# Kernel optimization log

Hardware: AMD Instinct MI355X
Metric: run time of the kernel (lower is better)

The kernel has to match this reference:

```python
import jax, jax.numpy as jnp
import numpy as np

CODEBOOK_SIZE = 4096
EMBED_DIM = 256
BETA = 0.25


def setup_inputs() -> dict:
    key = jax.random.key(0)
    k_z, k_cb = jax.random.split(key)
    z = jax.random.normal(k_z, (32, 256, 32, 32), dtype=jnp.float32)
    # nn.Embedding weight init: uniform(-1/D, 1/D)
    codebook = jax.random.uniform(
        k_cb, (CODEBOOK_SIZE, EMBED_DIM), dtype=jnp.float32,
        minval=-1.0 / EMBED_DIM, maxval=1.0 / EMBED_DIM)
    return {"z": z, "codebook": codebook}


def reference(z, codebook):
    b, c, h, w = z.shape
    # (B,C,H,W) -> (B*H*W, D)
    z_flat = jnp.transpose(z, (0, 2, 3, 1)).reshape(-1, c)
    # squared euclidean distances: ||z||^2 - 2 z.e^T + ||e||^2  (== cdist(...)^2)
    z_sq = jnp.sum(z_flat * z_flat, axis=1, keepdims=True)          # (N,1)
    e_sq = jnp.sum(codebook * codebook, axis=1)                     # (K,)
    distances = z_sq - 2.0 * (z_flat @ codebook.T) + e_sq[None, :]  # (N,K)
    min_encoding_indices = jnp.argmin(distances, axis=1)            # (N,)
    z_q_flat = codebook[min_encoding_indices]                       # (N,D)
    z_q = jnp.transpose(z_q_flat.reshape(b, h, w, c), (0, 3, 1, 2))  # (B,C,H,W)
    # straight-through estimator
    z_q_st = z + jax.lax.stop_gradient(z_q - z)
    codebook_loss = jnp.mean((z_q - jax.lax.stop_gradient(z)) ** 2)
    commitment_loss = jnp.mean((z - jax.lax.stop_gradient(z_q)) ** 2)
    vq_loss = codebook_loss + BETA * commitment_loss
    return (z_q_st, vq_loss, min_encoding_indices.reshape(b, h, w))
```

## Files before the change

### kernel.cpp

```cpp
#include <hip/hip_runtime.h>

#define K_CODES 4096
#define D 256
#define N_VEC 32768
#define N_ELEM 8388608
#define WINDOW 3.5e-4f
#define WINDOW_C 5.25e-4f
#define CAP 14
#define CSTRIDE 16
#define RG 8
#define RSLICE 256

typedef _Float16 f16x8 __attribute__((ext_vector_type(8)));
typedef float f32x4 __attribute__((ext_vector_type(4)));

#define WS_LOSS 0
#define WS_COUNT 8
#define WS_DONE 16
#define WS_COUNT2 24
#define WS_IDX 256
#define WS_LIST (WS_IDX + N_VEC * 4)
#define WS_ESQ (WS_LIST + N_VEC * 4)
#define WS_ZSQ (WS_ESQ + K_CODES * 4)
#define WS_APACK (WS_ZSQ + N_VEC * 4)
#define WS_BPACK (WS_APACK + (size_t)N_VEC * 256 * 2)
#define WS_RFIN (WS_BPACK + (size_t)K_CODES * 256 * 2 + 65536)
#define WS_ZT (WS_RFIN + (size_t)N_VEC * 8)
#define WS_NEED_ZT (WS_ZT + (size_t)N_VEC * D * 4)
#define WS_S1F WS_NEED_ZT
#define WS_CANDN (WS_S1F + (size_t)N_VEC * 4)
#define WS_CANDL (WS_CANDN + (size_t)N_VEC * 4)
#define WS_LISTB (WS_CANDL + (size_t)N_VEC * CSTRIDE * 2)
#define WS_NEED_CAND (WS_LISTB + (size_t)N_VEC * 4)

#define PREP_PZ 4096
#define PREP_PCB 512
#define PREP_ESQ 1024
#define PREP_ZSQ 128
#define PREP_BLOCKS (PREP_PZ + PREP_PCB + PREP_ESQ + PREP_ZSQ)

__device__ __forceinline__ unsigned long long pack_key(float s, int idx) {
  const unsigned u = __float_as_uint(s);
  const unsigned mk = (u & 0x80000000u) ? ~u : (u | 0x80000000u);
  return ((unsigned long long)mk << 12) | (unsigned long long)(unsigned)idx;
}
__device__ __forceinline__ float key_score(unsigned long long k) {
  const unsigned mk = (unsigned)(k >> 12);
  const unsigned u = (mk & 0x80000000u) ? (mk & 0x7fffffffu) : ~mk;
  return __uint_as_float(u);
}

__device__ __forceinline__ void pin_frag(f16x8& v) {
  asm volatile("" : "+v"(v));
}

__device__ void esq_body(int bx, const float* __restrict__ cb,
                         float* __restrict__ esq) {
  const int lane = threadIdx.x & 63;
  const int k = bx * 4 + (threadIdx.x >> 6);
  const float* row = cb + (size_t)k * D;
  double s = 0.;
#pragma unroll
  for (int j = 0; j < 4; ++j) {
    const float v = row[lane + 64 * j];
    s += (double)__fmul_rn(v, v);
  }
#pragma unroll
  for (int off = 32; off > 0; off >>= 1) s += __shfl_down(s, off, 64);
  if (lane == 0) esq[k] = (float)s;
}

__device__ void zsq_body(int bx, const float* __restrict__ z,
                         float* __restrict__ zsq) {
  const int n = bx * 256 + threadIdx.x;
  const int b = n >> 10;
  const int hw = n & 1023;
  const float* p = z + ((size_t)b << 18) + hw;
  double a0 = 0., a1 = 0., a2 = 0., a3 = 0.;
  for (int c = 0; c < D; c += 4) {
    const float v0 = p[(size_t)(c + 0) << 10];
    const float v1 = p[(size_t)(c + 1) << 10];
    const float v2 = p[(size_t)(c + 2) << 10];
    const float v3 = p[(size_t)(c + 3) << 10];
    a0 += (double)__fmul_rn(v0, v0);
    a1 += (double)__fmul_rn(v1, v1);
    a2 += (double)__fmul_rn(v2, v2);
    a3 += (double)__fmul_rn(v3, v3);
  }
  zsq[n] = (float)((a0 + a1) + (a2 + a3));
}

__device__ void pack_z2_body(int bx, const float* __restrict__ z,
                             _Float16* __restrict__ Ap,
                             float* __restrict__ zT) {
  const int t = bx * 256 + threadIdx.x;
  const int lane = t & 63;
  const int fid = t >> 6;
  const int ks = fid & 7;
  const int grp = fid >> 3;
  const int n = grp * 16 + (lane & 15);
  const int d = ks * 32 + ((lane >> 4) << 3);
  const int b = n >> 10, hw = n & 1023;
  const float* p = z + ((size_t)b << 18) + ((size_t)d << 10) + hw;
  float v[8];
  f16x8 H;
#pragma unroll
  for (int j = 0; j < 8; ++j) {
    v[j] = p[(size_t)j << 10];
    H[j] = (_Float16)v[j];
  }
  *(f16x8*)(Ap + (size_t)t * 8) = H;
  if (zT) {
    float4* o = (float4*)(zT + (size_t)n * D + d);
    o[0] = make_float4(v[0], v[1], v[2], v[3]);
    o[1] = make_float4(v[4], v[5], v[6], v[7]);
  }
}

__device__ void pack_cb2_body(int bx, const float* __restrict__ cb,
                              _Float16* __restrict__ Bp) {
  const int t = bx * 256 + threadIdx.x;
  const int lane = t & 63;
  const int fid = t >> 6;
  const int ks = fid & 7;
  const int grp = fid >> 3;
  const int k = grp * 16 + (lane & 15);
  const int d = ks * 32 + ((lane >> 4) << 3);
  const float* p = cb + (size_t)k * D + d;
  f16x8 H;
#pragma unroll
  for (int j = 0; j < 8; ++j) H[j] = (_Float16)(p[j] * 256.f);
  *(f16x8*)(Bp + (size_t)t * 8) = H;
}

__global__ __launch_bounds__(256) void prep_kernel(
    const float* __restrict__ z, const float* __restrict__ cb,
    float* __restrict__ esq, float* __restrict__ zsq,
    _Float16* __restrict__ Ap, _Float16* __restrict__ Bp,
    float* __restrict__ zT) {
  const int b = blockIdx.x;
  if (b < PREP_PZ) {
    pack_z2_body(b, z, Ap, zT);
  } else if (b < PREP_PZ + PREP_PCB) {
    pack_cb2_body(b - PREP_PZ, cb, Bp);
  } else if (b < PREP_PZ + PREP_PCB + PREP_ESQ) {
    esq_body(b - PREP_PZ - PREP_PCB, cb, esq);
  } else {
    zsq_body(b - PREP_PZ - PREP_PCB - PREP_ESQ, z, zsq);
  }
}

__global__ __launch_bounds__(512, 2) void dist2_kernel(
    const _Float16* __restrict__ Ap, const _Float16* __restrict__ Bp,
    const float* __restrict__ esq, int* __restrict__ idx,
    int* __restrict__ list, unsigned int* __restrict__ count,
    unsigned long long* __restrict__ rfin, float* __restrict__ s1f,
    int* __restrict__ listB, unsigned int* __restrict__ count2) {
  __shared__ unsigned long long mb[128][4][2];
  const int tid = threadIdx.x;
  const int lane = tid & 63;
  const int w = tid >> 6;
  const int wn = w >> 2;
  const int wc = w & 3;
  const int n0 = blockIdx.x * 128;

  f16x8 a[4][8];
  {
    const _Float16* ab =
        Ap + (size_t)((n0 + wn * 64) >> 4) * 4096 + (size_t)lane * 8;
#pragma unroll
    for (int ni = 0; ni < 4; ++ni)
#pragma unroll
      for (int ks = 0; ks < 8; ++ks) {
        a[ni][ks] = *(const f16x8*)(ab + (size_t)(ni * 8 + ks) * 512);
        pin_frag(a[ni][ks]);
      }
  }

  float s1[4], s2[4];
  int i1[4];
#pragma unroll
  for (int ni = 0; ni < 4; ++ni) {
    s1[ni] = 3.4e38f;
    s2[ni] = 3.4e38f;
    i1[ni] = 0;
  }

  const _Float16* bbase = Bp + (size_t)wc * 4096 + (size_t)lane * 8;
  const int crow = wc * 16 + ((lane >> 4) << 2);
  const f32x4 z4 = (f32x4)0.f;

  f16x8 b[8];
#pragma unroll
  for (int ks = 0; ks < 8; ++ks)
    b[ks] = *(const f16x8*)(bbase + (size_t)ks * 512);

  for (int t = 0; t < 64; ++t) {
    const float4 e4 = *(const float4*)(esq + t * 64 + crow);
    f32x4 acc0, acc1, acc2, acc3;
    __builtin_amdgcn_s_setprio(1);
#pragma unroll
    for (int ks = 0; ks < 8; ++ks) {
      acc0 = __builtin_amdgcn_mfma_f32_16x16x32_f16(b[ks], a[0][ks],
                                                    ks ? acc0 : z4, 0, 0, 0);
      acc1 = __builtin_amdgcn_mfma_f32_16x16x32_f16(b[ks], a[1][ks],
                                                    ks ? acc1 : z4, 0, 0, 0);
      acc2 = __builtin_amdgcn_mfma_f32_16x16x32_f16(b[ks], a[2][ks],
                                                    ks ? acc2 : z4, 0, 0, 0);
      acc3 = __builtin_amdgcn_mfma_f32_16x16x32_f16(b[ks], a[3][ks],
                                                    ks ? acc3 : z4, 0, 0, 0);
      b[ks] = *(const f16x8*)(bbase + (size_t)(t + 1) * 16384 + ks * 512);
    }
    __builtin_amdgcn_s_setprio(0);
    const int cb0 = t * 64 + crow;
    const float ev[4] = {e4.x, e4.y, e4.z, e4.w};
    f32x4 accv[4] = {acc0, acc1, acc2, acc3};
#pragma unroll
    for (int r = 0; r < 4; ++r) {
      const int code = cb0 + r;
#pragma unroll
      for (int ni = 0; ni < 4; ++ni) {
        const float s = fmaf(accv[ni][r], -0.0078125f, ev[r]);
        s2[ni] = fminf(fmaxf(s, s1[ni]), s2[ni]);
        if (s < s1[ni]) i1[ni] = code;
        s1[ni] = fminf(s1[ni], s);
      }
    }
  }

  unsigned long long k1[4], k2[4];
#pragma unroll
  for (int ni = 0; ni < 4; ++ni) {
    float a1 = s1[ni], a2 = s2[ni];
    int ai1 = i1[ni];
#pragma unroll
    for (int m = 16; m <= 32; m <<= 1) {
      const float bv1 = __shfl_xor(a1, m, 64);
      const int bi1 = __shfl_xor(ai1, m, 64);
      const float bv2 = __shfl_xor(a2, m, 64);
      const float hi = fmaxf(a1, bv1);
      const bool take = (bv1 < a1) || (bv1 == a1 && bi1 < ai1);
      if (take) ai1 = bi1;
      a1 = fminf(a1, bv1);
      a2 = fminf(fminf(a2, bv2), hi);
    }
    k1[ni] = pack_key(a1, ai1);
    k2[ni] = pack_key(a2, 0);
  }
  if (lane < 16) {
#pragma unroll
    for (int ni = 0; ni < 4; ++ni) {
      const int nl = wn * 64 + ni * 16 + lane;
      mb[nl][wc][0] = k1[ni];
      mb[nl][wc][1] = k2[ni];
    }
  }
  __syncthreads();
  if (tid < 128) {
    unsigned long long m1 = ~0ull, m2 = ~0ull;
#pragma unroll
    for (int s = 0; s < 4; ++s) {
      const unsigned long long c1 = mb[tid][s][0];
      const unsigned long long c2 = mb[tid][s][1];
      if (c1 < m1) {
        m2 = m1;
        m1 = c1;
      } else if (c1 < m2) {
        m2 = c1;
      }
      if (c2 < m2) m2 = c2;
    }
    const int n = n0 + tid;
    idx[n] = (int)(m1 & 0xFFFULL);
    const float sc0 = key_score(m1);
    if (s1f) s1f[n] = sc0;
    const bool flag = key_score(m2) - sc0 < WINDOW;
    rfin[n] = flag ? ~0ull : 0ull;
    if (flag) {
      if (s1f) {
        const unsigned pos = atomicAdd(count, 1u);
        if (pos < N_VEC) list[pos] = n;
      } else {
        const unsigned p2 = atomicAdd(count2, 1u);
        if (p2 < N_VEC) listB[p2] = n;
      }
    }
  }
}

__global__ __launch_bounds__(64) void certify_kernel(
    const _Float16* __restrict__ Ap, const _Float16* __restrict__ Bp,
    const float* __restrict__ esq, const float* __restrict__ s1f,
    const int* __restrict__ list, const unsigned int* __restrict__ count,
    unsigned int* __restrict__ candn, unsigned short* __restrict__ candl) {
  if (!candn) return;
  unsigned int cN = *count;
  if (cN > N_VEC) cN = N_VEC;
  if (cN == 0) return;
  const int lane = threadIdx.x & 63;
  const int l16 = lane & 15;
  const int quad = lane >> 4;
  const unsigned ptiles = (cN + 15) / 16;
  const unsigned items = ptiles * 16;
  const f32x4 z4 = (f32x4)0.f;
  for (unsigned item = blockIdx.x; item < items; item += gridDim.x) {
    const unsigned pt = item >> 4;
    const unsigned sl = item & 15;
    unsigned r = pt * 16 + l16;
    const bool valid = (r < cN);
    if (!valid) r = cN - 1;
    const int n = list[r];
    const float thr = s1f[n] + WINDOW_C;
    f16x8 af[8];
    const _Float16* ab = Ap + (size_t)(n >> 4) * 4096 + (size_t)quad * 128 +
                         (size_t)(n & 15) * 8;
#pragma unroll
    for (int ks = 0; ks < 8; ++ks) {
      af[ks] = *(const f16x8*)(ab + (size_t)ks * 512);
      pin_frag(af[ks]);
    }
#pragma unroll 2
    for (int g = 0; g < 16; ++g) {
      const int grp = sl * 16 + g;
      const _Float16* bb = Bp + (size_t)grp * 4096 + (size_t)lane * 8;
      f16x8 bf[8];
#pragma unroll
      for (int ks = 0; ks < 8; ++ks)
        bf[ks] = *(const f16x8*)(bb + (size_t)ks * 512);
      f32x4 acc;
#pragma unroll
      for (int ks = 0; ks < 8; ++ks)
        acc = __builtin_amdgcn_mfma_f32_16x16x32_f16(bf[ks], af[ks],
                                                     ks ? acc : z4, 0, 0, 0);
      const int cb0 = grp * 16 + quad * 4;
      const float4 e4 = *(const float4*)(esq + cb0);
      const float ev[4] = {e4.x, e4.y, e4.z, e4.w};
#pragma unroll
      for (int rr = 0; rr < 4; ++rr) {
        const float s = fmaf(acc[rr], -0.0078125f, ev[rr]);
        if (valid && s < thr) {
          const unsigned u = atomicAdd(&candn[n], 1u);
          if (u < CAP)
            candl[(size_t)n * CSTRIDE + u] = (unsigned short)(cb0 + rr);
        }
      }
    }
  }
}

__global__ __launch_bounds__(256) void rescanB_kernel(
    const float* __restrict__ zT, const float* __restrict__ cb,
    const float* __restrict__ esq, const float* __restrict__ zsq,
    const int* __restrict__ list, const unsigned int* __restrict__ count,
    const unsigned int* __restrict__ candn,
    const unsigned short* __restrict__ candl,
    unsigned long long* __restrict__ rfin, int* __restrict__ listB,
    unsigned int* __restrict__ count2) {
  if (!candn) return;
  unsigned int cN = *count;
  if (cN > N_VEC) cN = N_VEC;
  const int tid = threadIdx.x;
  const int j8 = tid & 7;
  for (unsigned i = blockIdx.x * 32 + (tid >> 3); i < cN;
       i += gridDim.x * 32) {
    const int n = list[i];
    const unsigned c = candn[n];
    if (c > CAP) {
      if (j8 == 0) {
        const unsigned p = atomicAdd(count2, 1u);
        if (p < N_VEC) listB[p] = n;
      }
      continue;
    }
    unsigned long long best = ~0ull;
    for (unsigned jj = j8; jj < c; jj += 8) {
      const int k = candl[(size_t)n * CSTRIDE + jj];
      const float* zr = zT + (size_t)n * D;
      const float* row = cb + (size_t)k * D;
      double a = 0.;
      for (int cc = 0; cc < D; cc += 4) {
        const float4 zf = *(const float4*)(zr + cc);
        const float4 r4 = *(const float4*)(row + cc);
        a = fma((double)zf.x, (double)r4.x, a);
        a = fma((double)zf.y, (double)r4.y, a);
        a = fma((double)zf.z, (double)r4.z, a);
        a = fma((double)zf.w, (double)r4.w, a);
      }
      const float d =
          __fadd_rn(__fsub_rn(zsq[n], __fmul_rn(2.0f, (float)a)), esq[k]);
      best = min(best, pack_key(d, k));
    }
    best = min(best, __shfl_xor(best, 1, 64));
    best = min(best, __shfl_xor(best, 2, 64));
    best = min(best, __shfl_xor(best, 4, 64));
    if (j8 == 0 && best != ~0ull) atomicMin(rfin + n, best);
  }
}

__global__ __launch_bounds__(256) void rescan_kernel(
    const float* __restrict__ z, const float* __restrict__ zT,
    const float* __restrict__ cb, const float* __restrict__ esq,
    const float* __restrict__ zsq, const int* __restrict__ list,
    const unsigned int* __restrict__ count,
    unsigned long long* __restrict__ rfin) {
  __shared__ double zrow[RG][D];
  __shared__ int nloc[RG];
  __shared__ float zsv[RG];
  const int tid = threadIdx.x;
  const int lane = tid & 63;
  unsigned int cnt = *count;
  if (cnt > N_VEC) cnt = N_VEC;
  const unsigned G = (cnt + RG - 1) / RG;
  const unsigned nitems = G * (K_CODES / RSLICE);
  for (unsigned item = blockIdx.x; item < nitems; item += gridDim.x) {
    const unsigned g = item >> 4;
    const int s = item & 15;
    __syncthreads();
    if (tid < RG) {
      const unsigned r = g * RG + tid;
      const int n = (r < cnt) ? list[r] : list[cnt - 1];
      nloc[tid] = n;
      zsv[tid] = zsq[n];
    }
    __syncthreads();
    if (zT) {
      for (int i = tid; i < RG * D; i += 256) {
        const int p = i >> 8, c = i & 255;
        zrow[p][c] = (double)zT[(size_t)nloc[p] * D + c];
      }
    } else {
      for (int i = tid; i < RG * D; i += 256) {
        const int p = i >> 8, c = i & 255;
        const int n = nloc[p];
        const int b = n >> 10, hw = n & 1023;
        zrow[p][c] = (double)z[((size_t)b << 18) + ((size_t)c << 10) + hw];
      }
    }
    __syncthreads();
    const int k = s * RSLICE + tid;
    const float* row = cb + (size_t)k * D;
    double acc[RG];
#pragma unroll
    for (int p = 0; p < RG; ++p) acc[p] = 0.;
    for (int c = 0; c < D; c += 4) {
      const float4 r4 = *(const float4*)(row + c);
      const double rx = (double)r4.x, ry = (double)r4.y;
      const double rz = (double)r4.z, rw = (double)r4.w;
#pragma unroll
      for (int p = 0; p < RG; ++p) {
        const double2 za = *(const double2*)&zrow[p][c];
        const double2 zb = *(const double2*)&zrow[p][c + 2];
        double a = acc[p];
        a = fma(za.x, rx, a);
        a = fma(za.y, ry, a);
        a = fma(zb.x, rz, a);
        a = fma(zb.y, rw, a);
        acc[p] = a;
      }
    }
    const float ek = esq[k];
    unsigned long long best[RG];
#pragma unroll
    for (int p = 0; p < RG; ++p) {
      const float dotf = (float)acc[p];
      const float d = __fadd_rn(__fsub_rn(zsv[p], __fmul_rn(2.0f, dotf)), ek);
      best[p] = pack_key(d, k);
    }
#pragma unroll
    for (int p = 0; p < RG; ++p) {
#pragma unroll
      for (int off = 32; off > 0; off >>= 1)
        best[p] = min(best[p], __shfl_down(best[p], off, 64));
    }
    if (lane == 0) {
#pragma unroll
      for (int p = 0; p < RG; ++p) atomicMin(rfin + nloc[p], best[p]);
    }
  }
}

__global__ __launch_bounds__(256) void gather_kernel(
    const float* __restrict__ z, const float* __restrict__ cb,
    const int* __restrict__ idxarr, const unsigned long long* __restrict__ rfin,
    float* __restrict__ out, float* __restrict__ loss_acc,
    unsigned int* __restrict__ done) {
  const int tid = threadIdx.x;
  const int n0 = blockIdx.x * 64;
  const int hwl = tid & 63;
  const int cq = tid >> 6;
  const int n = n0 + hwl;
  const int b = n >> 10;
  const int hw = n & 1023;
  const unsigned long long rf = rfin[n];
  const int idx = rf ? (int)(rf & 0xFFFULL) : idxarr[n];
  if (tid < 64) out[(size_t)N_ELEM + 1 + n] = (float)idx;
  const float* crow = cb + (size_t)idx * D;
  const size_t obase = ((size_t)b << 18) + hw;
  float part = 0.f;
#pragma unroll
  for (int j = 0; j < 16; ++j) {
    const int c = cq * 64 + j * 4;
    const float4 v4 = *(const float4*)(crow + c);
    const size_t o = obase + ((size_t)c << 10);
    const float d0 = v4.x - z[o];
    const float d1 = v4.y - z[o + 1024];
    const float d2 = v4.z - z[o + 2048];
    const float d3 = v4.w - z[o + 3072];
    out[o] = v4.x;
    out[o + 1024] = v4.y;
    out[o + 2048] = v4.z;
    out[o + 3072] = v4.w;
    part = fmaf(d0, d0, part);
    part = fmaf(d1, d1, part);
    part = fmaf(d2, d2, part);
    part = fmaf(d3, d3, part);
  }
#pragma unroll
  for (int off = 32; off > 0; off >>= 1) part += __shfl_down(part, off, 64);
  __shared__ float red[4];
  if ((tid & 63) == 0) red[tid >> 6] = part;
  __syncthreads();
  if (tid == 0) {
    atomicAdd(loss_acc, red[0] + red[1] + red[2] + red[3]);
    __threadfence();
    const unsigned old = atomicAdd(done, 1u);
    if (old == gridDim.x - 1) {
      const float total = atomicAdd(loss_acc, 0.0f);
      out[N_ELEM] = 1.25f * total * (1.0f / (float)N_ELEM);
    }
  }
}

extern "C" void kernel_launch(void* const* d_in, const int* in_sizes, int n_in,
                              void* d_out, int out_size, void* d_ws,
                              size_t ws_size, hipStream_t stream) {
  const float* z = (const float*)d_in[0];
  const float* cb = (const float*)d_in[1];
  float* out = (float*)d_out;
  char* ws = (char*)d_ws;
  float* loss_acc = (float*)(ws + WS_LOSS);
  unsigned int* count = (unsigned int*)(ws + WS_COUNT);
  unsigned int* done = (unsigned int*)(ws + WS_DONE);
  unsigned int* count2 = (unsigned int*)(ws + WS_COUNT2);
  int* idx = (int*)(ws + WS_IDX);
  int* list = (int*)(ws + WS_LIST);
  float* esq = (float*)(ws + WS_ESQ);
  float* zsq = (float*)(ws + WS_ZSQ);
  _Float16* Ap = (_Float16*)(ws + WS_APACK);
  _Float16* Bp = (_Float16*)(ws + WS_BPACK);
  unsigned long long* rfin = (unsigned long long*)(ws + WS_RFIN);
  float* zT = (ws_size >= WS_NEED_ZT) ? (float*)(ws + WS_ZT) : nullptr;
  const bool canduse = (ws_size >= WS_NEED_CAND) && (zT != nullptr);
  float* s1f = canduse ? (float*)(ws + WS_S1F) : nullptr;
  unsigned int* candn = canduse ? (unsigned int*)(ws + WS_CANDN) : nullptr;
  unsigned short* candl = canduse ? (unsigned short*)(ws + WS_CANDL) : nullptr;
  int* listB = canduse ? (int*)(ws + WS_LISTB) : list;

  hipMemsetAsync(ws, 0, 256, stream);
  if (canduse) hipMemsetAsync(ws + WS_CANDN, 0, (size_t)N_VEC * 4, stream);
  prep_kernel<<<PREP_BLOCKS, 256, 0, stream>>>(z, cb, esq, zsq, Ap, Bp, zT);
  dist2_kernel<<<N_VEC / 128, 512, 0, stream>>>(Ap, Bp, esq, idx, list, count,
                                                rfin, s1f, listB, count2);
  certify_kernel<<<2048, 64, 0, stream>>>(Ap, Bp, esq, s1f, list, count, candn,
                                          candl);
  rescanB_kernel<<<256, 256, 0, stream>>>(zT, cb, esq, zsq, list, count, candn,
                                          candl, rfin, listB, count2);
  rescan_kernel<<<2048, 256, 0, stream>>>(z, zT, cb, esq, zsq, listB, count2,
                                          rfin);
  gather_kernel<<<N_VEC / 64, 256, 0, stream>>>(z, cb, idx, rfin, out,
                                                loss_acc, done);
}
```

Measured before the change: 249.0 us.

## Fuse candidate certification and exact rescan into one block-local kernel

Replaces the separate certify, rescanB and rescan kernels with a single cresolve kernel. Each block takes 16 ambiguous vectors, recomputes their approximate fp16 MFMA distances against the whole codebook, and collects near-minimum candidates in shared memory. It then resolves them exactly in double precision, falling back to a full in-block scan when a vector has too many candidates. This removes the zT transpose buffer, the global candidate arrays and their memset, atomics, and extra launches, but each block now does all 4096-code MFMA work serially and can hit a costly full-scan path.

```diff
diff --git a/kernel.cpp b/kernel.cpp
--- a/kernel.cpp
+++ b/kernel.cpp
@@ -6,8 +6,7 @@
 #define N_ELEM 8388608
 #define WINDOW 3.5e-4f
 #define WINDOW_C 5.25e-4f
-#define CAP 14
-#define CSTRIDE 16
+#define CAP2 30
 #define RG 8
 #define RSLICE 256
 
@@ -25,13 +24,8 @@
 #define WS_APACK (WS_ZSQ + N_VEC * 4)
 #define WS_BPACK (WS_APACK + (size_t)N_VEC * 256 * 2)
 #define WS_RFIN (WS_BPACK + (size_t)K_CODES * 256 * 2 + 65536)
-#define WS_ZT (WS_RFIN + (size_t)N_VEC * 8)
-#define WS_NEED_ZT (WS_ZT + (size_t)N_VEC * D * 4)
-#define WS_S1F WS_NEED_ZT
-#define WS_CANDN (WS_S1F + (size_t)N_VEC * 4)
-#define WS_CANDL (WS_CANDN + (size_t)N_VEC * 4)
-#define WS_LISTB (WS_CANDL + (size_t)N_VEC * CSTRIDE * 2)
-#define WS_NEED_CAND (WS_LISTB + (size_t)N_VEC * 4)
+#define WS_S1F (WS_RFIN + (size_t)N_VEC * 8)
+#define WS_NEED_CERT (WS_S1F + (size_t)N_VEC * 4)
 
 #define PREP_PZ 4096
 #define PREP_PCB 512
@@ -288,112 +282,147 @@
   }
 }
 
-__global__ __launch_bounds__(64) void certify_kernel(
+__global__ __launch_bounds__(512) void cresolve_kernel(
     const _Float16* __restrict__ Ap, const _Float16* __restrict__ Bp,
-    const float* __restrict__ esq, const float* __restrict__ s1f,
-    const int* __restrict__ list, const unsigned int* __restrict__ count,
-    unsigned int* __restrict__ candn, unsigned short* __restrict__ candl) {
-  if (!candn) return;
+    const float* __restrict__ cb, const float* __restrict__ esq,
+    const float* __restrict__ zsq, const float* __restrict__ s1f,
+    const float* __restrict__ z, const int* __restrict__ list,
+    const unsigned int* __restrict__ count,
+    unsigned long long* __restrict__ rfin) {
+  __shared__ float zrow[16][260];
+  __shared__ int nloc[16];
+  __shared__ float thrs[16];
+  __shared__ unsigned int lcnt[16];
+  __shared__ unsigned short lcodes[16][CAP2 + 2];
+  __shared__ unsigned long long mb2[16][32];
   unsigned int cN = *count;
   if (cN > N_VEC) cN = N_VEC;
   if (cN == 0) return;
-  const int lane = threadIdx.x & 63;
+  const int tid = threadIdx.x;
+  const int lane = tid & 63;
+  const int w = tid >> 6;
   const int l16 = lane & 15;
   const int quad = lane >> 4;
   const unsigned ptiles = (cN + 15) / 16;
-  const unsigned items = ptiles * 16;
   const f32x4 z4 = (f32x4)0.f;
-  for (unsigned item = blockIdx.x; item < items; item += gridDim.x) {
-    const unsigned pt = item >> 4;
-    const unsigned sl = item & 15;
-    unsigned r = pt * 16 + l16;
-    const bool valid = (r < cN);
-    if (!valid) r = cN - 1;
-    const int n = list[r];
-    const float thr = s1f[n] + WINDOW_C;
-    f16x8 af[8];
-    const _Float16* ab = Ap + (size_t)(n >> 4) * 4096 + (size_t)quad * 128 +
-                         (size_t)(n & 15) * 8;
-#pragma unroll
-    for (int ks = 0; ks < 8; ++ks) {
-      af[ks] = *(const f16x8*)(ab + (size_t)ks * 512);
-      pin_frag(af[ks]);
-    }
+  for (unsigned pt = blockIdx.x; pt < ptiles; pt += gridDim.x) {
+    __syncthreads();
+    if (tid < 16) {
+      unsigned r = pt * 16 + tid;
+      if (r >= cN) r = cN - 1;
+      const int n = list[r];
+      nloc[tid] = n;
+      thrs[tid] = s1f[n] + WINDOW_C;
+      lcnt[tid] = 0;
+    }
+    __syncthreads();
+    {
+      const int p = tid >> 5;
+      const int n = nloc[p];
+      const int b = n >> 10, hw = n & 1023;
+      const float* zp = z + ((size_t)b << 18) + hw;
+      for (int c = tid & 31; c < 256; c += 32)
+        zrow[p][c] = zp[(size_t)c << 10];
+    }
+    {
+      const int n = nloc[l16];
+      const float thr = thrs[l16];
+      f16x8 af[8];
+      const _Float16* ab = Ap + (size_t)(n >> 4) * 4096 +
+                           (size_t)quad * 128 + (size_t)(n & 15) * 8;
+#pragma unroll
+      for (int ks = 0; ks < 8; ++ks) {
+        af[ks] = *(const f16x8*)(ab + (size_t)ks * 512);
+        pin_frag(af[ks]);
+      }
 #pragma unroll 2
-    for (int g = 0; g < 16; ++g) {
-      const int grp = sl * 16 + g;
-      const _Float16* bb = Bp + (size_t)grp * 4096 + (size_t)lane * 8;
-      f16x8 bf[8];
-#pragma unroll
-      for (int ks = 0; ks < 8; ++ks)
-        bf[ks] = *(const f16x8*)(bb + (size_t)ks * 512);
-      f32x4 acc;
-#pragma unroll
-      for (int ks = 0; ks < 8; ++ks)
-        acc = __builtin_amdgcn_mfma_f32_16x16x32_f16(bf[ks], af[ks],
-                                                     ks ? acc : z4, 0, 0, 0);
-      const int cb0 = grp * 16 + quad * 4;
-      const float4 e4 = *(const float4*)(esq + cb0);
-      const float ev[4] = {e4.x, e4.y, e4.z, e4.w};
-#pragma unroll
-      for (int rr = 0; rr < 4; ++rr) {
-        const float s = fmaf(acc[rr], -0.0078125f, ev[rr]);
-        if (valid && s < thr) {
-          const unsigned u = atomicAdd(&candn[n], 1u);
-          if (u < CAP)
-            candl[(size_t)n * CSTRIDE + u] = (unsigned short)(cb0 + rr);
+      for (int j = 0; j < 32; ++j) {
+        const int grp = j * 8 + w;
+        const _Float16* bb = Bp + (size_t)grp * 4096 + (size_t)lane * 8;
+        f16x8 bf[8];
+#pragma unroll
+        for (int ks = 0; ks < 8; ++ks)
+          bf[ks] = *(const f16x8*)(bb + (size_t)ks * 512);
+        f32x4 acc;
+#pragma unroll
+        for (int ks = 0; ks < 8; ++ks)
+          acc = __builtin_amdgcn_mfma_f32_16x16x32_f16(bf[ks], af[ks],
+                                                       ks ? acc : z4, 0, 0, 0);
+        const int cb0 = grp * 16 + quad * 4;
+        const float4 e4 = *(const float4*)(esq + cb0);
+        const float ev[4] = {e4.x, e4.y, e4.z, e4.w};
+#pragma unroll
+        for (int rr = 0; rr < 4; ++rr) {
+          const float s = fmaf(acc[rr], -0.0078125f, ev[rr]);
+          if (s < thr) {
+            const unsigned u = atomicAdd(&lcnt[l16], 1u);
+            if (u < CAP2) lcodes[l16][u] = (unsigned short)(cb0 + rr);
+          }
         }
       }
     }
-  }
-}
-
-__global__ __launch_bounds__(256) void rescanB_kernel(
-    const float* __restrict__ zT, const float* __restrict__ cb,
-    const float* __restrict__ esq, const float* __restrict__ zsq,
-    const int* __restrict__ list, const unsigned int* __restrict__ count,
-    const unsigned int* __restrict__ candn,
-    const unsigned short* __restrict__ candl,
-    unsigned long long* __restrict__ rfin, int* __restrict__ listB,
-    unsigned int* __restrict__ count2) {
-  if (!candn) return;
-  unsigned int cN = *count;
-  if (cN > N_VEC) cN = N_VEC;
-  const int tid = threadIdx.x;
-  const int j8 = tid & 7;
-  for (unsigned i = blockIdx.x * 32 + (tid >> 3); i < cN;
-       i += gridDim.x * 32) {
-    const int n = list[i];
-    const unsigned c = candn[n];
-    if (c > CAP) {
-      if (j8 == 0) {
-        const unsigned p = atomicAdd(count2, 1u);
-        if (p < N_VEC) listB[p] = n;
-      }
-      continue;
-    }
-    unsigned long long best = ~0ull;
-    for (unsigned jj = j8; jj < c; jj += 8) {
-      const int k = candl[(size_t)n * CSTRIDE + jj];
-      const float* zr = zT + (size_t)n * D;
-      const float* row = cb + (size_t)k * D;
-      double a = 0.;
-      for (int cc = 0; cc < D; cc += 4) {
-        const float4 zf = *(const float4*)(zr + cc);
-        const float4 r4 = *(const float4*)(row + cc);
-        a = fma((double)zf.x, (double)r4.x, a);
-        a = fma((double)zf.y, (double)r4.y, a);
-        a = fma((double)zf.z, (double)r4.z, a);
-        a = fma((double)zf.w, (double)r4.w, a);
-      }
-      const float d =
-          __fadd_rn(__fsub_rn(zsq[n], __fmul_rn(2.0f, (float)a)), esq[k]);
-      best = min(best, pack_key(d, k));
-    }
-    best = min(best, __shfl_xor(best, 1, 64));
-    best = min(best, __shfl_xor(best, 2, 64));
-    best = min(best, __shfl_xor(best, 4, 64));
-    if (j8 == 0 && best != ~0ull) atomicMin(rfin + n, best);
+    __syncthreads();
+    {
+      const int p = tid >> 5;
+      const int jj = tid & 31;
+      const unsigned c = lcnt[p];
+      unsigned long long key = ~0ull;
+      if (jj < (int)c && jj < CAP2) {
+        const int k = lcodes[p][jj];
+        const float* row = cb + (size_t)k * D;
+        double a = 0.;
+        for (int cc = 0; cc < D; cc += 4) {
+          const float4 r4 = *(const float4*)(row + cc);
+          a = fma((double)zrow[p][cc + 0], (double)r4.x, a);
+          a = fma((double)zrow[p][cc + 1], (double)r4.y, a);
+          a = fma((double)zrow[p][cc + 2], (double)r4.z, a);
+          a = fma((double)zrow[p][cc + 3], (double)r4.w, a);
+        }
+        const float d = __fadd_rn(
+            __fsub_rn(zsq[nloc[p]], __fmul_rn(2.0f, (float)a)), esq[k]);
+        key = pack_key(d, k);
+      }
+      mb2[p][jj] = key;
+    }
+    __syncthreads();
+    if (tid < 16) {
+      const unsigned c = lcnt[tid];
+      if (c <= CAP2) {
+        unsigned long long best = ~0ull;
+#pragma unroll
+        for (int j = 0; j < 32; ++j) best = min(best, mb2[tid][j]);
+        rfin[nloc[tid]] = best;
+      }
+    }
+    __syncthreads();
+    for (int p2 = 0; p2 < 16; ++p2) {
+      if (lcnt[p2] <= CAP2) continue;
+      const int n2 = nloc[p2];
+      unsigned long long bt = ~0ull;
+      for (int k = tid; k < K_CODES; k += 512) {
+        const float* row = cb + (size_t)k * D;
+        double a = 0.;
+        for (int cc = 0; cc < D; cc += 4) {
+          const float4 r4 = *(const float4*)(row + cc);
+          a = fma((double)zrow[p2][cc + 0], (double)r4.x, a);
+          a = fma((double)zrow[p2][cc + 1], (double)r4.y, a);
+          a = fma((double)zrow[p2][cc + 2], (double)r4.z, a);
+          a = fma((double)zrow[p2][cc + 3], (double)r4.w, a);
+        }
+        const float d = __fadd_rn(
+            __fsub_rn(zsq[n2], __fmul_rn(2.0f, (float)a)), esq[k]);
+        bt = min(bt, pack_key(d, k));
+      }
+      unsigned long long* fb = &mb2[0][0];
+      fb[tid] = bt;
+      __syncthreads();
+      for (int s = 256; s > 0; s >>= 1) {
+        if (tid < s) fb[tid] = min(fb[tid], fb[tid + s]);
+        __syncthreads();
+      }
+      if (tid == 0) rfin[n2] = fb[0];
+      __syncthreads();
+    }
   }
 }
 
@@ -549,24 +578,21 @@
   _Float16* Ap = (_Float16*)(ws + WS_APACK);
   _Float16* Bp = (_Float16*)(ws + WS_BPACK);
   unsigned long long* rfin = (unsigned long long*)(ws + WS_RFIN);
-  float* zT = (ws_size >= WS_NEED_ZT) ? (float*)(ws + WS_ZT) : nullptr;
-  const bool canduse = (ws_size >= WS_NEED_CAND) && (zT != nullptr);
-  float* s1f = canduse ? (float*)(ws + WS_S1F) : nullptr;
-  unsigned int* candn = canduse ? (unsigned int*)(ws + WS_CANDN) : nullptr;
-  unsigned short* candl = canduse ? (unsigned short*)(ws + WS_CANDL) : nullptr;
-  int* listB = canduse ? (int*)(ws + WS_LISTB) : list;
+  const bool certuse = (ws_size >= WS_NEED_CERT);
+  float* s1f = certuse ? (float*)(ws + WS_S1F) : nullptr;
 
   hipMemsetAsync(ws, 0, 256, stream);
-  if (canduse) hipMemsetAsync(ws + WS_CANDN, 0, (size_t)N_VEC * 4, stream);
-  prep_kernel<<<PREP_BLOCKS, 256, 0, stream>>>(z, cb, esq, zsq, Ap, Bp, zT);
+  prep_kernel<<<PREP_BLOCKS, 256, 0, stream>>>(z, cb, esq, zsq, Ap, Bp,
+                                               nullptr);
   dist2_kernel<<<N_VEC / 128, 512, 0, stream>>>(Ap, Bp, esq, idx, list, count,
-                                                rfin, s1f, listB, count2);
-  certify_kernel<<<2048, 64, 0, stream>>>(Ap, Bp, esq, s1f, list, count, candn,
-                                          candl);
-  rescanB_kernel<<<256, 256, 0, stream>>>(zT, cb, esq, zsq, list, count, candn,
-                                          candl, rfin, listB, count2);
-  rescan_kernel<<<2048, 256, 0, stream>>>(z, zT, cb, esq, zsq, listB, count2,
-                                          rfin);
+                                                rfin, s1f, list, count2);
+  if (certuse) {
+    cresolve_kernel<<<256, 512, 0, stream>>>(Ap, Bp, cb, esq, zsq, s1f, z,
+                                             list, count, rfin);
+  } else {
+    rescan_kernel<<<2048, 256, 0, stream>>>(z, nullptr, cb, esq, zsq, list,
+                                            count2, rfin);
+  }
   gather_kernel<<<N_VEC / 64, 256, 0, stream>>>(z, cb, idx, rfin, out,
                                                 loss_acc, done);
 }
```

Result: slower. 271.9 us (+9.2%).

## Split distance GEMM over codebook halves and merge top-2 in a separate kernel

Applied to the files above, without the earlier changes.

The distance kernel now launches twice as many blocks, each scanning half of the codebook (32 of 64 tiles) for a 128-vector tile, and writes per-half best and second-best packed keys to a new workspace buffer. A new merge kernel combines the two halves' top-2 keys and does the index, margin flag, and candidate-list work the distance kernel used to do. This doubles the grid (256 to 512 blocks) to fill more CUs on the GPU. The cost is an extra kernel launch, a candp round trip through global memory, and reloading the A fragments in both halves. The certify and rescanB launches are now skipped when the candidate workspace is unavailable.

```diff
diff --git a/kernel.cpp b/kernel.cpp
--- a/kernel.cpp
+++ b/kernel.cpp
@@ -25,7 +25,8 @@
 #define WS_APACK (WS_ZSQ + N_VEC * 4)
 #define WS_BPACK (WS_APACK + (size_t)N_VEC * 256 * 2)
 #define WS_RFIN (WS_BPACK + (size_t)K_CODES * 256 * 2 + 65536)
-#define WS_ZT (WS_RFIN + (size_t)N_VEC * 8)
+#define WS_CANDP (WS_RFIN + (size_t)N_VEC * 8)
+#define WS_ZT (WS_CANDP + (size_t)4 * N_VEC * 8)
 #define WS_NEED_ZT (WS_ZT + (size_t)N_VEC * D * 4)
 #define WS_S1F WS_NEED_ZT
 #define WS_CANDN (WS_S1F + (size_t)N_VEC * 4)
@@ -152,17 +153,16 @@
 
 __global__ __launch_bounds__(512, 2) void dist2_kernel(
     const _Float16* __restrict__ Ap, const _Float16* __restrict__ Bp,
-    const float* __restrict__ esq, int* __restrict__ idx,
-    int* __restrict__ list, unsigned int* __restrict__ count,
-    unsigned long long* __restrict__ rfin, float* __restrict__ s1f,
-    int* __restrict__ listB, unsigned int* __restrict__ count2) {
+    const float* __restrict__ esq, unsigned long long* __restrict__ candp) {
   __shared__ unsigned long long mb[128][4][2];
   const int tid = threadIdx.x;
   const int lane = tid & 63;
   const int w = tid >> 6;
   const int wn = w >> 2;
   const int wc = w & 3;
-  const int n0 = blockIdx.x * 128;
+  const int n0 = (blockIdx.x >> 1) * 128;
+  const int kh = blockIdx.x & 1;
+  const int t0 = kh * 32;
 
   f16x8 a[4][8];
   {
@@ -193,9 +193,9 @@
   f16x8 b[8];
 #pragma unroll
   for (int ks = 0; ks < 8; ++ks)
-    b[ks] = *(const f16x8*)(bbase + (size_t)ks * 512);
-
-  for (int t = 0; t < 64; ++t) {
+    b[ks] = *(const f16x8*)(bbase + (size_t)t0 * 16384 + ks * 512);
+
+  for (int t = t0; t < t0 + 32; ++t) {
     const float4 e4 = *(const float4*)(esq + t * 64 + crow);
     f32x4 acc0, acc1, acc2, acc3;
     __builtin_amdgcn_s_setprio(1);
@@ -270,20 +270,36 @@
       }
       if (c2 < m2) m2 = c2;
     }
-    const int n = n0 + tid;
-    idx[n] = (int)(m1 & 0xFFFULL);
-    const float sc0 = key_score(m1);
-    if (s1f) s1f[n] = sc0;
-    const bool flag = key_score(m2) - sc0 < WINDOW;
-    rfin[n] = flag ? ~0ull : 0ull;
-    if (flag) {
-      if (s1f) {
-        const unsigned pos = atomicAdd(count, 1u);
-        if (pos < N_VEC) list[pos] = n;
-      } else {
-        const unsigned p2 = atomicAdd(count2, 1u);
-        if (p2 < N_VEC) listB[p2] = n;
-      }
+    const size_t n = n0 + tid;
+    candp[(size_t)(kh * 2 + 0) * N_VEC + n] = m1;
+    candp[(size_t)(kh * 2 + 1) * N_VEC + n] = m2;
+  }
+}
+
+__global__ __launch_bounds__(256) void merge2_kernel(
+    const unsigned long long* __restrict__ candp, int* __restrict__ idx,
+    float* __restrict__ s1f, unsigned long long* __restrict__ rfin,
+    int* __restrict__ list, unsigned int* __restrict__ count,
+    int* __restrict__ listB, unsigned int* __restrict__ count2) {
+  const int n = blockIdx.x * 256 + threadIdx.x;
+  const unsigned long long a1 = candp[(size_t)0 * N_VEC + n];
+  const unsigned long long a2 = candp[(size_t)1 * N_VEC + n];
+  const unsigned long long b1 = candp[(size_t)2 * N_VEC + n];
+  const unsigned long long b2 = candp[(size_t)3 * N_VEC + n];
+  const unsigned long long m1 = min(a1, b1);
+  const unsigned long long m2 = min(max(a1, b1), min(a2, b2));
+  idx[n] = (int)(m1 & 0xFFFULL);
+  const float sc0 = key_score(m1);
+  if (s1f) s1f[n] = sc0;
+  const bool flag = key_score(m2) - sc0 < WINDOW;
+  rfin[n] = flag ? ~0ull : 0ull;
+  if (flag) {
+    if (s1f) {
+      const unsigned pos = atomicAdd(count, 1u);
+      if (pos < N_VEC) list[pos] = n;
+    } else {
+      const unsigned p2 = atomicAdd(count2, 1u);
+      if (p2 < N_VEC) listB[p2] = n;
     }
   }
 }
@@ -549,6 +565,7 @@
   _Float16* Ap = (_Float16*)(ws + WS_APACK);
   _Float16* Bp = (_Float16*)(ws + WS_BPACK);
   unsigned long long* rfin = (unsigned long long*)(ws + WS_RFIN);
+  unsigned long long* candp = (unsigned long long*)(ws + WS_CANDP);
   float* zT = (ws_size >= WS_NEED_ZT) ? (float*)(ws + WS_ZT) : nullptr;
   const bool canduse = (ws_size >= WS_NEED_CAND) && (zT != nullptr);
   float* s1f = canduse ? (float*)(ws + WS_S1F) : nullptr;
@@ -559,12 +576,15 @@
   hipMemsetAsync(ws, 0, 256, stream);
   if (canduse) hipMemsetAsync(ws + WS_CANDN, 0, (size_t)N_VEC * 4, stream);
   prep_kernel<<<PREP_BLOCKS, 256, 0, stream>>>(z, cb, esq, zsq, Ap, Bp, zT);
-  dist2_kernel<<<N_VEC / 128, 512, 0, stream>>>(Ap, Bp, esq, idx, list, count,
-                                                rfin, s1f, listB, count2);
-  certify_kernel<<<2048, 64, 0, stream>>>(Ap, Bp, esq, s1f, list, count, candn,
-                                          candl);
-  rescanB_kernel<<<256, 256, 0, stream>>>(zT, cb, esq, zsq, list, count, candn,
-                                          candl, rfin, listB, count2);
+  dist2_kernel<<<N_VEC / 64, 512, 0, stream>>>(Ap, Bp, esq, candp);
+  merge2_kernel<<<N_VEC / 256, 256, 0, stream>>>(candp, idx, s1f, rfin, list,
+                                                 count, listB, count2);
+  if (canduse) {
+    certify_kernel<<<2048, 64, 0, stream>>>(Ap, Bp, esq, s1f, list, count,
+                                            candn, candl);
+    rescanB_kernel<<<256, 256, 0, stream>>>(zT, cb, esq, zsq, list, count,
+                                            candn, candl, rfin, listB, count2);
+  }
   rescan_kernel<<<2048, 256, 0, stream>>>(z, zT, cb, esq, zsq, listB, count2,
                                           rfin);
   gather_kernel<<<N_VEC / 64, 256, 0, stream>>>(z, cb, idx, rfin, out,
```

Result: slower. 261.7 us (+5.1%).
